# Kernel tuning notes

Hardware: AMD Instinct MI355X
Metric: run time of the kernel (lower is better)

## Reference

```python
import jax, jax.numpy as jnp
import numpy as np

B, T, I, H, O = 128, 1024, 256, 1024, 128


def setup_inputs() -> dict:
    key = jax.random.key(0)
    ks = jax.random.split(key, 7)
    s = 1.0 / np.sqrt(H)  # PyTorch GRUCell init scale
    return {
        "sequence": jax.random.normal(ks[0], (B, T, I), dtype=jnp.float32),
        "W_ih": jax.random.uniform(ks[1], (3 * H, I), jnp.float32, -s, s),
        "W_hh": jax.random.uniform(ks[2], (3 * H, H), jnp.float32, -s, s),
        "b_ih": jax.random.uniform(ks[3], (3 * H,), jnp.float32, -s, s),
        "b_hh": jax.random.uniform(ks[4], (3 * H,), jnp.float32, -s, s),
        "W_out": jax.random.uniform(ks[5], (O, H), jnp.float32, -s, s),
        "b_out": jax.random.uniform(ks[6], (O,), jnp.float32, -s, s),
    }


def reference(sequence, W_ih, W_hh, b_ih, b_hh, W_out, b_out):
    Bs, Ts, _ = sequence.shape
    Hs = W_hh.shape[1]

    def step(h, x_t):
        gi = x_t @ W_ih.T + b_ih            # [B, 3H]
        gh = h @ W_hh.T + b_hh              # [B, 3H]
        i_r, i_z, i_n = jnp.split(gi, 3, axis=1)
        h_r, h_z, h_n = jnp.split(gh, 3, axis=1)
        r = jax.nn.sigmoid(i_r + h_r)
        z = jax.nn.sigmoid(i_z + h_z)
        n = jnp.tanh(i_n + r * h_n)
        h_new = (1.0 - z) * n + z * h       # PyTorch GRUCell update
        out = jax.nn.log_softmax(h_new @ W_out.T + b_out, axis=1)
        return h_new, out

    xs = jnp.swapaxes(sequence[:, : Ts - 1, :], 0, 1)  # [T-1, B, I]
    h0 = jnp.zeros((Bs, Hs), dtype=sequence.dtype)     # init_hx = zeros
    _, outs = jax.lax.scan(step, h0, xs)               # [T-1, B, O]
    return jnp.swapaxes(outs, 0, 1)                    # [B, T-1, O]
```

## Files before the change

### kernel.cpp

```cpp
#include <hip/hip_runtime.h>


typedef __attribute__((ext_vector_type(8))) __bf16 bf16x8;
typedef __attribute__((ext_vector_type(4))) float floatx4;
typedef __attribute__((ext_vector_type(8))) unsigned short ushortx8;
typedef unsigned short ushort_t;
typedef unsigned int uint_t;
typedef unsigned long long ull_t;

#define T_ 1024
#define I_ 256

#define NWPACK   3932160
#define NWOPACK  131072
#define HPACK_SLOT 131072
#define WPACK_OFF   0
#define WOPACK_OFF  (NWPACK*2)
#define HPACK_OFF   (WOPACK_OFF + NWOPACK*2)
#define OUTPART_OFF (HPACK_OFF + 4*HPACK_SLOT*2)
#define BAR_OFF     (OUTPART_OFF + 131072*4)

__device__ __forceinline__ ushort_t f2bf(float f) {
    uint_t u = __float_as_uint(f);
    u += 0x7fffu + ((u >> 16) & 1u);
    return (ushort_t)(u >> 16);
}

__device__ __forceinline__ floatx4 mfma16(bf16x8 a, bf16x8 b, floatx4 c) {
    return __builtin_amdgcn_mfma_f32_16x16x32_bf16(a, b, c, 0, 0, 0);
}

__device__ __forceinline__ bf16x8 ld_llc16(const ushort_t* p) {
    union { ull_t q[2]; bf16x8 v; } u;
    u.q[0] = __hip_atomic_load((const ull_t*)p,     __ATOMIC_RELAXED, __HIP_MEMORY_SCOPE_AGENT);
    u.q[1] = __hip_atomic_load((const ull_t*)p + 1, __ATOMIC_RELAXED, __HIP_MEMORY_SCOPE_AGENT);
    return u.v;
}
__device__ __forceinline__ void st_llc2(ushort_t* p, ushort_t v) {
    __hip_atomic_store(p, v, __ATOMIC_RELAXED, __HIP_MEMORY_SCOPE_AGENT);
}
__device__ __forceinline__ void st_llc4f(float* p, float v) {
    __hip_atomic_store(p, v, __ATOMIC_RELAXED, __HIP_MEMORY_SCOPE_AGENT);
}
__device__ __forceinline__ float ld_llc4f(const float* p) {
    return __hip_atomic_load(p, __ATOMIC_RELAXED, __HIP_MEMORY_SCOPE_AGENT);
}

__global__ void gru_init(const float* __restrict__ W_ih, const float* __restrict__ W_hh,
                         const float* __restrict__ W_out,
                         ushort_t* __restrict__ wpack, ushort_t* __restrict__ wopack,
                         ushort_t* __restrict__ hpack0, uint_t* __restrict__ bar)
{
    const int total = NWPACK + NWOPACK + HPACK_SLOT/2 + 1024;
    for (int e = blockIdx.x * 256 + threadIdx.x; e < total; e += gridDim.x * 256) {
        if (e < NWPACK) {
            int j = e & 7;
            int lane = (e >> 3) & 63;
            int t2 = e >> 9;
            int g  = t2 % 3;
            int t3 = t2 / 3;
            int kb = t3 % 40;
            int cg = t3 / 40;
            int n = g * 1024 + cg * 16 + (lane & 15);
            int koff = ((lane >> 4) << 3) + j;
            float v;
            if (kb < 8) v = W_ih[(size_t)n * 256 + kb * 32 + koff];
            else        v = W_hh[(size_t)n * 1024 + (kb - 8) * 32 + koff];
            wpack[e] = f2bf(v);
        } else if (e < NWPACK + NWOPACK) {
            int e2 = e - NWPACK;
            int j = e2 & 7;
            int lane = (e2 >> 3) & 63;
            int kb = (e2 >> 9) & 31;
            int nt = e2 >> 14;
            int n = nt * 16 + (lane & 15);
            int k = kb * 32 + ((lane >> 4) << 3) + j;
            wopack[e2] = f2bf(W_out[(size_t)n * 1024 + k]);
        } else if (e < NWPACK + NWOPACK + HPACK_SLOT/2) {
            ((uint_t*)hpack0)[e - NWPACK - NWOPACK] = 0u;
        } else {
            bar[e - NWPACK - NWOPACK - HPACK_SLOT/2] = 0u;
        }
    }
}

__device__ __forceinline__ void group_barrier(uint_t* bar, int grp, uint_t target)
{
    __syncthreads();
    if (threadIdx.x == 0) {
        uint_t* cnt = bar + grp * 64;
        uint_t* gen = bar + grp * 64 + 32;
        uint_t a = __hip_atomic_fetch_add(cnt, 1u, __ATOMIC_RELAXED, __HIP_MEMORY_SCOPE_AGENT);
        if (a == (target << 6) - 1u) {
            __hip_atomic_fetch_add(gen, 1u, __ATOMIC_RELAXED, __HIP_MEMORY_SCOPE_AGENT);
        } else {
            while (__hip_atomic_load(gen, __ATOMIC_RELAXED, __HIP_MEMORY_SCOPE_AGENT) < target)
                __builtin_amdgcn_s_sleep(1);
        }
    }
    __syncthreads();
}

__global__ void __launch_bounds__(256, 1)
gru_main(const float* __restrict__ seq,
         const float* __restrict__ b_ih, const float* __restrict__ b_hh,
         const float* __restrict__ b_out,
         const ushort_t* __restrict__ wpack, const ushort_t* __restrict__ wopack,
         ushort_t* __restrict__ hpack, float* __restrict__ outpart,
         uint_t* __restrict__ bar, float* __restrict__ dout)
{
    extern __shared__ char lds[];
    ushort_t* wlds = (ushort_t*)lds;
    float*    xch  = (float*)(lds + 122880);

    const int b   = blockIdx.x;
    const int grp = (b & 7) >> 1;
    const int id  = ((b >> 3) << 1) | (b & 1);
    const int cg  = id;
    const int m   = grp;
    const int tid = threadIdx.x;
    const int wv  = tid >> 6;
    const int ln  = tid & 63;

    {
        const uint4* src = (const uint4*)(wpack + (size_t)cg * 61440);
        uint4* dst = (uint4*)lds;
        for (int i = tid; i < 7680; i += 256) dst[i] = src[i];
    }

    float bihr = 0, bhhr = 0, bihz = 0, bhhz = 0, bihn = 0, bhhn = 0;
    if (wv < 2) {
        int col = cg * 16 + (ln & 15);
        bihr = b_ih[col];          bhhr = b_hh[col];
        bihz = b_ih[1024 + col];   bhhz = b_hh[1024 + col];
        bihn = b_ih[2048 + col];   bhhn = b_hh[2048 + col];
    }
    const float bo0 = b_out[ln], bo1 = b_out[ln + 64];

    floatx4 hold = {0.f, 0.f, 0.f, 0.f};

    const int omt = 2 * grp + (id & 1);
    const int ont = (id >> 1) & 7;
    const int oks = (id >> 4) & 3;
    const int kb0 = wv * 10;
    const int mtb0 = m * 2, mtb1 = m * 2 + 1;

    __syncthreads();

#define XSLOT(sw, mt, g) (xch + (((sw) * 2 + (mt)) * 4 + (g)) * 256 + ln * 4)

    for (int it = 0; it < 1025; ++it) {
        const ushort_t* hcur = hpack + (size_t)(it & 3) * HPACK_SLOT;

        floatx4 accr0 = {0,0,0,0}, accr1 = {0,0,0,0};
        floatx4 accz0 = {0,0,0,0}, accz1 = {0,0,0,0};
        floatx4 acch0 = {0,0,0,0}, acch1 = {0,0,0,0};
        floatx4 acci0 = {0,0,0,0}, acci1 = {0,0,0,0};

        if (it <= 1022) {
            #pragma unroll
            for (int ki = 0; ki < 10; ++ki) {
                const int kb = kb0 + ki;
                bf16x8 a0, a1;
                if (kb < 8) {
                    int koffx = kb * 32 + ((ln >> 4) << 3);
                    const float* p0 = seq + (size_t)(mtb0 * 16 + (ln & 15)) * (T_ * I_)
                                          + (size_t)it * I_ + koffx;
                    const float* p1 = p0 + (size_t)16 * (T_ * I_);
                    float4 fa = *(const float4*)p0, fb = *(const float4*)(p0 + 4);
                    float4 ga = *(const float4*)p1, gb = *(const float4*)(p1 + 4);
                    ushortx8 u0, u1;
                    u0[0] = f2bf(fa.x); u0[1] = f2bf(fa.y); u0[2] = f2bf(fa.z); u0[3] = f2bf(fa.w);
                    u0[4] = f2bf(fb.x); u0[5] = f2bf(fb.y); u0[6] = f2bf(fb.z); u0[7] = f2bf(fb.w);
                    u1[0] = f2bf(ga.x); u1[1] = f2bf(ga.y); u1[2] = f2bf(ga.z); u1[3] = f2bf(ga.w);
                    u1[4] = f2bf(gb.x); u1[5] = f2bf(gb.y); u1[6] = f2bf(gb.z); u1[7] = f2bf(gb.w);
                    a0 = __builtin_bit_cast(bf16x8, u0);
                    a1 = __builtin_bit_cast(bf16x8, u1);
                } else {
                    a0 = ld_llc16(hcur + (((size_t)mtb0 * 32 + (kb - 8)) * 64 + ln) * 8);
                    a1 = ld_llc16(hcur + (((size_t)mtb1 * 32 + (kb - 8)) * 64 + ln) * 8);
                }
                const bf16x8 br = *(const bf16x8*)(wlds + ((kb * 3 + 0) * 64 + ln) * 8);
                const bf16x8 bz = *(const bf16x8*)(wlds + ((kb * 3 + 1) * 64 + ln) * 8);
                const bf16x8 bn = *(const bf16x8*)(wlds + ((kb * 3 + 2) * 64 + ln) * 8);
                accr0 = mfma16(a0, br, accr0);  accr1 = mfma16(a1, br, accr1);
                accz0 = mfma16(a0, bz, accz0);  accz1 = mfma16(a1, bz, accz1);
                if (kb < 8) { acci0 = mfma16(a0, bn, acci0); acci1 = mfma16(a1, bn, acci1); }
                else        { acch0 = mfma16(a0, bn, acch0); acch1 = mfma16(a1, bn, acch1); }
            }
            if (wv == 0) {
                *(floatx4*)XSLOT(0, 1, 0) = accr1; *(floatx4*)XSLOT(0, 1, 1) = accz1;
                *(floatx4*)XSLOT(0, 1, 2) = acch1; *(floatx4*)XSLOT(0, 1, 3) = acci1;
            } else if (wv == 1) {
                *(floatx4*)XSLOT(1, 0, 0) = accr0; *(floatx4*)XSLOT(1, 0, 1) = accz0;
                *(floatx4*)XSLOT(1, 0, 2) = acch0;
            } else {
                *(floatx4*)XSLOT(wv, 0, 0) = accr0; *(floatx4*)XSLOT(wv, 0, 1) = accz0;
                *(floatx4*)XSLOT(wv, 0, 2) = acch0;
                *(floatx4*)XSLOT(wv, 1, 0) = accr1; *(floatx4*)XSLOT(wv, 1, 1) = accz1;
                *(floatx4*)XSLOT(wv, 1, 2) = acch1;
            }
        }
        __syncthreads();

        if (it <= 1022 && wv < 2) {
            const int mtr = wv;
            floatx4 r  = (mtr == 0) ? accr0 : accr1;
            floatx4 z  = (mtr == 0) ? accz0 : accz1;
            floatx4 hn = (mtr == 0) ? acch0 : acch1;
            floatx4 inn = (wv == 0) ? acci0 : *(floatx4*)XSLOT(0, 1, 3);
            #pragma unroll
            for (int sw = 0; sw < 4; ++sw) {
                if (sw == wv) continue;
                r  += *(floatx4*)XSLOT(sw, mtr, 0);
                z  += *(floatx4*)XSLOT(sw, mtr, 1);
                hn += *(floatx4*)XSLOT(sw, mtr, 2);
            }
            ushort_t* hnew = hpack + (size_t)((it + 1) & 3) * HPACK_SLOT;
            const int mtW = m * 2 + mtr;
            const int kbh = cg >> 1;
            const int koffb = ((cg & 1) << 4) + (ln & 15);
            const int lanep = (koffb >> 3) << 4;
            const int jj = koffb & 7;
            const int rbase = (ln >> 4) * 4;
            #pragma unroll
            for (int e = 0; e < 4; ++e) {
                float rp = r[e] + bihr + bhhr;
                float rg = 1.f / (1.f + __expf(-rp));
                float zp = z[e] + bihz + bhhz;
                float zg = 1.f / (1.f + __expf(-zp));
                float nx = inn[e] + bihn + rg * (hn[e] + bhhn);
                float ng = 1.f - 2.f / (__expf(2.f * nx) + 1.f);
                float hv = (1.f - zg) * ng + zg * hold[e];
                hold[e] = hv;
                size_t idx = (((size_t)mtW * 32 + kbh) * 64 + (unsigned)((rbase + e) | lanep)) * 8 + jj;
                st_llc2(&hnew[idx], f2bf(hv));
            }
        }

        if (wv == 2 && it >= 1 && it <= 1023) {
            const ushort_t* hh = hpack + (size_t)(it & 3) * HPACK_SLOT;
            floatx4 acc = {0, 0, 0, 0};
            #pragma unroll
            for (int i2 = 0; i2 < 8; ++i2) {
                int kb = oks * 8 + i2;
                bf16x8 a = ld_llc16(hh + (((size_t)omt * 32 + kb) * 64 + ln) * 8);
                bf16x8 bb = *(const bf16x8*)(wopack + (((size_t)ont * 32 + kb) * 64 + ln) * 8);
                acc = mfma16(a, bb, acc);
            }
            float* op = outpart + (size_t)(it & 1) * 65536 + (size_t)oks * 16384;
            int colo = ont * 16 + (ln & 15);
            #pragma unroll
            for (int e = 0; e < 4; ++e) {
                int rowo = omt * 16 + (ln >> 4) * 4 + e;
                st_llc4f(op + rowo * 128 + colo, acc[e]);
            }
        }

        if (wv == 3 && id < 32 && it >= 2) {
            const float* op = outpart + (size_t)((it - 1) & 1) * 65536;
            const int row = grp * 32 + id;
            float v0 = bo0, v1 = bo1;
            #pragma unroll
            for (int ks2 = 0; ks2 < 4; ++ks2) {
                v0 += ld_llc4f(op + ks2 * 16384 + row * 128 + ln);
                v1 += ld_llc4f(op + ks2 * 16384 + row * 128 + ln + 64);
            }
            float mx = fmaxf(v0, v1);
            #pragma unroll
            for (int off = 32; off >= 1; off >>= 1) mx = fmaxf(mx, __shfl_xor(mx, off));
            float e0 = __expf(v0 - mx), e1 = __expf(v1 - mx);
            float sm = e0 + e1;
            #pragma unroll
            for (int off = 32; off >= 1; off >>= 1) sm += __shfl_xor(sm, off);
            float lse = mx + __logf(sm);
            float* po = dout + ((size_t)row * 1023 + (it - 2)) * 128;
            po[ln] = v0 - lse;
            po[ln + 64] = v1 - lse;
        }

        if (it < 1024) group_barrier(bar, grp, (uint_t)(it + 1));
    }
#undef XSLOT
}

extern "C" void kernel_launch(void* const* d_in, const int* in_sizes, int n_in,
                              void* d_out, int out_size, void* d_ws, size_t ws_size,
                              hipStream_t stream)
{
    const float* seq  = (const float*)d_in[0];
    const float* Wih  = (const float*)d_in[1];
    const float* Whh  = (const float*)d_in[2];
    const float* bih  = (const float*)d_in[3];
    const float* bhh  = (const float*)d_in[4];
    const float* Wout = (const float*)d_in[5];
    const float* bout = (const float*)d_in[6];

    char* ws = (char*)d_ws;
    ushort_t* wpack   = (ushort_t*)(ws + WPACK_OFF);
    ushort_t* wopack  = (ushort_t*)(ws + WOPACK_OFF);
    ushort_t* hpack   = (ushort_t*)(ws + HPACK_OFF);
    float*    outpart = (float*)(ws + OUTPART_OFF);
    uint_t*   bar     = (uint_t*)(ws + BAR_OFF);

    gru_init<<<1024, 256, 0, stream>>>(Wih, Whh, Wout, wpack, wopack, hpack, bar);

    hipFuncSetAttribute((const void*)gru_main,
                        hipFuncAttributeMaxDynamicSharedMemorySize, 155648);
    gru_main<<<256, 256, 155648, stream>>>(seq, bih, bhh, bout, wpack, wopack,
                                           hpack, outpart, bar, (float*)d_out);
}
```

Baseline: 9.504 ms.

## Replace group barrier with per-wave counter waits and overlap input projection

Replaces the full block-level group barrier with a monotonically increasing per-group counter: the two gate waves increment it after their hidden-state stores drain, and every wave polls it individually only before consuming the new hidden state. The input-projection MFMAs and the output-projection partials are hoisted ahead of the wait, so they overlap with the cross-block synchronization. The new hidden state is staged in LDS and written as 64-bit stores instead of scattered 16-bit stores. The output pipeline is deepened to four buffers to tolerate the looser coupling. The cost is extra LDS space and more complex memory-ordering assumptions, with relaxed atomics and an explicit vmcnt wait.

```diff
diff --git a/kernel.cpp b/kernel.cpp
--- a/kernel.cpp
+++ b/kernel.cpp
@@ -18,7 +18,7 @@
 #define WOPACK_OFF  (NWPACK*2)
 #define HPACK_OFF   (WOPACK_OFF + NWOPACK*2)
 #define OUTPART_OFF (HPACK_OFF + 4*HPACK_SLOT*2)
-#define BAR_OFF     (OUTPART_OFF + 131072*4)
+#define BAR_OFF     (OUTPART_OFF + 4*65536*4)
 
 __device__ __forceinline__ ushort_t f2bf(float f) {
     uint_t u = __float_as_uint(f);
@@ -36,7 +36,7 @@
     u.q[1] = __hip_atomic_load((const ull_t*)p + 1, __ATOMIC_RELAXED, __HIP_MEMORY_SCOPE_AGENT);
     return u.v;
 }
-__device__ __forceinline__ void st_llc2(ushort_t* p, ushort_t v) {
+__device__ __forceinline__ void st_llc8(ull_t* p, ull_t v) {
     __hip_atomic_store(p, v, __ATOMIC_RELAXED, __HIP_MEMORY_SCOPE_AGENT);
 }
 __device__ __forceinline__ void st_llc4f(float* p, float v) {
@@ -84,21 +84,14 @@
     }
 }
 
-__device__ __forceinline__ void group_barrier(uint_t* bar, int grp, uint_t target)
+__device__ __forceinline__ void wave_wait(uint_t* cnt, uint_t target, int ln)
 {
-    __syncthreads();
-    if (threadIdx.x == 0) {
-        uint_t* cnt = bar + grp * 64;
-        uint_t* gen = bar + grp * 64 + 32;
-        uint_t a = __hip_atomic_fetch_add(cnt, 1u, __ATOMIC_RELAXED, __HIP_MEMORY_SCOPE_AGENT);
-        if (a == (target << 6) - 1u) {
-            __hip_atomic_fetch_add(gen, 1u, __ATOMIC_RELAXED, __HIP_MEMORY_SCOPE_AGENT);
-        } else {
-            while (__hip_atomic_load(gen, __ATOMIC_RELAXED, __HIP_MEMORY_SCOPE_AGENT) < target)
-                __builtin_amdgcn_s_sleep(1);
-        }
-    }
-    __syncthreads();
+    if (ln == 0) {
+        while (__hip_atomic_load(cnt, __ATOMIC_RELAXED, __HIP_MEMORY_SCOPE_AGENT) < target)
+            __builtin_amdgcn_s_sleep(1);
+    }
+    __builtin_amdgcn_wave_barrier();
+    asm volatile("" ::: "memory");
 }
 
 __global__ void __launch_bounds__(256, 1)
@@ -112,6 +105,7 @@
     extern __shared__ char lds[];
     ushort_t* wlds = (ushort_t*)lds;
     float*    xch  = (float*)(lds + 122880);
+    ushort_t* hsc  = (ushort_t*)(lds + 155648);
 
     const int b   = blockIdx.x;
     const int grp = (b & 7) >> 1;
@@ -121,6 +115,7 @@
     const int tid = threadIdx.x;
     const int wv  = tid >> 6;
     const int ln  = tid & 63;
+    uint_t* cnt = bar + grp * 64;
 
     {
         const uint4* src = (const uint4*)(wpack + (size_t)cg * 61440);
@@ -142,16 +137,13 @@
     const int omt = 2 * grp + (id & 1);
     const int ont = (id >> 1) & 7;
     const int oks = (id >> 4) & 3;
-    const int kb0 = wv * 10;
     const int mtb0 = m * 2, mtb1 = m * 2 + 1;
 
     __syncthreads();
 
 #define XSLOT(sw, mt, g) (xch + (((sw) * 2 + (mt)) * 4 + (g)) * 256 + ln * 4)
 
-    for (int it = 0; it < 1025; ++it) {
-        const ushort_t* hcur = hpack + (size_t)(it & 3) * HPACK_SLOT;
-
+    for (int it = 0; it < 1026; ++it) {
         floatx4 accr0 = {0,0,0,0}, accr1 = {0,0,0,0};
         floatx4 accz0 = {0,0,0,0}, accz1 = {0,0,0,0};
         floatx4 acch0 = {0,0,0,0}, acch1 = {0,0,0,0};
@@ -159,47 +151,91 @@
 
         if (it <= 1022) {
             #pragma unroll
-            for (int ki = 0; ki < 10; ++ki) {
-                const int kb = kb0 + ki;
-                bf16x8 a0, a1;
-                if (kb < 8) {
-                    int koffx = kb * 32 + ((ln >> 4) << 3);
-                    const float* p0 = seq + (size_t)(mtb0 * 16 + (ln & 15)) * (T_ * I_)
-                                          + (size_t)it * I_ + koffx;
-                    const float* p1 = p0 + (size_t)16 * (T_ * I_);
-                    float4 fa = *(const float4*)p0, fb = *(const float4*)(p0 + 4);
-                    float4 ga = *(const float4*)p1, gb = *(const float4*)(p1 + 4);
-                    ushortx8 u0, u1;
-                    u0[0] = f2bf(fa.x); u0[1] = f2bf(fa.y); u0[2] = f2bf(fa.z); u0[3] = f2bf(fa.w);
-                    u0[4] = f2bf(fb.x); u0[5] = f2bf(fb.y); u0[6] = f2bf(fb.z); u0[7] = f2bf(fb.w);
-                    u1[0] = f2bf(ga.x); u1[1] = f2bf(ga.y); u1[2] = f2bf(ga.z); u1[3] = f2bf(ga.w);
-                    u1[4] = f2bf(gb.x); u1[5] = f2bf(gb.y); u1[6] = f2bf(gb.z); u1[7] = f2bf(gb.w);
-                    a0 = __builtin_bit_cast(bf16x8, u0);
-                    a1 = __builtin_bit_cast(bf16x8, u1);
-                } else {
-                    a0 = ld_llc16(hcur + (((size_t)mtb0 * 32 + (kb - 8)) * 64 + ln) * 8);
-                    a1 = ld_llc16(hcur + (((size_t)mtb1 * 32 + (kb - 8)) * 64 + ln) * 8);
-                }
+            for (int ki = 0; ki < 2; ++ki) {
+                const int kb = wv * 2 + ki;
+                int koffx = kb * 32 + ((ln >> 4) << 3);
+                const float* p0 = seq + (size_t)(mtb0 * 16 + (ln & 15)) * (T_ * I_)
+                                      + (size_t)it * I_ + koffx;
+                const float* p1 = p0 + (size_t)16 * (T_ * I_);
+                float4 fa = *(const float4*)p0, fb = *(const float4*)(p0 + 4);
+                float4 ga = *(const float4*)p1, gb = *(const float4*)(p1 + 4);
+                ushortx8 u0, u1;
+                u0[0] = f2bf(fa.x); u0[1] = f2bf(fa.y); u0[2] = f2bf(fa.z); u0[3] = f2bf(fa.w);
+                u0[4] = f2bf(fb.x); u0[5] = f2bf(fb.y); u0[6] = f2bf(fb.z); u0[7] = f2bf(fb.w);
+                u1[0] = f2bf(ga.x); u1[1] = f2bf(ga.y); u1[2] = f2bf(ga.z); u1[3] = f2bf(ga.w);
+                u1[4] = f2bf(gb.x); u1[5] = f2bf(gb.y); u1[6] = f2bf(gb.z); u1[7] = f2bf(gb.w);
+                bf16x8 a0 = __builtin_bit_cast(bf16x8, u0);
+                bf16x8 a1 = __builtin_bit_cast(bf16x8, u1);
                 const bf16x8 br = *(const bf16x8*)(wlds + ((kb * 3 + 0) * 64 + ln) * 8);
                 const bf16x8 bz = *(const bf16x8*)(wlds + ((kb * 3 + 1) * 64 + ln) * 8);
                 const bf16x8 bn = *(const bf16x8*)(wlds + ((kb * 3 + 2) * 64 + ln) * 8);
                 accr0 = mfma16(a0, br, accr0);  accr1 = mfma16(a1, br, accr1);
                 accz0 = mfma16(a0, bz, accz0);  accz1 = mfma16(a1, bz, accz1);
-                if (kb < 8) { acci0 = mfma16(a0, bn, acci0); acci1 = mfma16(a1, bn, acci1); }
-                else        { acch0 = mfma16(a0, bn, acch0); acch1 = mfma16(a1, bn, acch1); }
-            }
-            if (wv == 0) {
-                *(floatx4*)XSLOT(0, 1, 0) = accr1; *(floatx4*)XSLOT(0, 1, 1) = accz1;
-                *(floatx4*)XSLOT(0, 1, 2) = acch1; *(floatx4*)XSLOT(0, 1, 3) = acci1;
-            } else if (wv == 1) {
-                *(floatx4*)XSLOT(1, 0, 0) = accr0; *(floatx4*)XSLOT(1, 0, 1) = accz0;
-                *(floatx4*)XSLOT(1, 0, 2) = acch0;
-            } else {
-                *(floatx4*)XSLOT(wv, 0, 0) = accr0; *(floatx4*)XSLOT(wv, 0, 1) = accz0;
-                *(floatx4*)XSLOT(wv, 0, 2) = acch0;
-                *(floatx4*)XSLOT(wv, 1, 0) = accr1; *(floatx4*)XSLOT(wv, 1, 1) = accz1;
-                *(floatx4*)XSLOT(wv, 1, 2) = acch1;
-            }
+                acci0 = mfma16(a0, bn, acci0);  acci1 = mfma16(a1, bn, acci1);
+            }
+        }
+
+        if (wv == 2 && it >= 2 && it <= 1024) {
+            const ushort_t* hh = hpack + (size_t)((it - 1) & 3) * HPACK_SLOT;
+            floatx4 acc = {0, 0, 0, 0};
+            #pragma unroll
+            for (int i2 = 0; i2 < 8; ++i2) {
+                int kb = oks * 8 + i2;
+                bf16x8 a = ld_llc16(hh + (((size_t)omt * 32 + kb) * 64 + ln) * 8);
+                bf16x8 bb = *(const bf16x8*)(wopack + (((size_t)ont * 32 + kb) * 64 + ln) * 8);
+                acc = mfma16(a, bb, acc);
+            }
+            float* op = outpart + (size_t)(it & 3) * 65536 + (size_t)oks * 16384;
+            int colo = ont * 16 + (ln & 15);
+            #pragma unroll
+            for (int e = 0; e < 4; ++e) {
+                int rowo = omt * 16 + (ln >> 4) * 4 + e;
+                st_llc4f(op + rowo * 128 + colo, acc[e]);
+            }
+        }
+
+        wave_wait(cnt, (uint_t)it * 128u, ln);
+
+        if (wv == 3 && id < 32 && it >= 3) {
+            const float* op = outpart + (size_t)((it - 1) & 3) * 65536;
+            const int row = grp * 32 + id;
+            float v0 = bo0, v1 = bo1;
+            #pragma unroll
+            for (int ks2 = 0; ks2 < 4; ++ks2) {
+                v0 += ld_llc4f(op + ks2 * 16384 + row * 128 + ln);
+                v1 += ld_llc4f(op + ks2 * 16384 + row * 128 + ln + 64);
+            }
+            float mx = fmaxf(v0, v1);
+            #pragma unroll
+            for (int off = 32; off >= 1; off >>= 1) mx = fmaxf(mx, __shfl_xor(mx, off));
+            float e0 = __expf(v0 - mx), e1 = __expf(v1 - mx);
+            float sm = e0 + e1;
+            #pragma unroll
+            for (int off = 32; off >= 1; off >>= 1) sm += __shfl_xor(sm, off);
+            float lse = mx + __logf(sm);
+            float* po = dout + ((size_t)row * 1023 + (it - 3)) * 128;
+            po[ln] = v0 - lse;
+            po[ln + 64] = v1 - lse;
+        }
+
+        if (it <= 1022) {
+            const ushort_t* hcur = hpack + (size_t)(it & 3) * HPACK_SLOT;
+            #pragma unroll
+            for (int ki = 0; ki < 8; ++ki) {
+                const int kb = 8 + wv * 8 + ki;
+                bf16x8 a0 = ld_llc16(hcur + (((size_t)mtb0 * 32 + (kb - 8)) * 64 + ln) * 8);
+                bf16x8 a1 = ld_llc16(hcur + (((size_t)mtb1 * 32 + (kb - 8)) * 64 + ln) * 8);
+                const bf16x8 br = *(const bf16x8*)(wlds + ((kb * 3 + 0) * 64 + ln) * 8);
+                const bf16x8 bz = *(const bf16x8*)(wlds + ((kb * 3 + 1) * 64 + ln) * 8);
+                const bf16x8 bn = *(const bf16x8*)(wlds + ((kb * 3 + 2) * 64 + ln) * 8);
+                accr0 = mfma16(a0, br, accr0);  accr1 = mfma16(a1, br, accr1);
+                accz0 = mfma16(a0, bz, accz0);  accz1 = mfma16(a1, bz, accz1);
+                acch0 = mfma16(a0, bn, acch0);  acch1 = mfma16(a1, bn, acch1);
+            }
+            *(floatx4*)XSLOT(wv, 0, 0) = accr0; *(floatx4*)XSLOT(wv, 0, 1) = accz0;
+            *(floatx4*)XSLOT(wv, 0, 2) = acch0; *(floatx4*)XSLOT(wv, 0, 3) = acci0;
+            *(floatx4*)XSLOT(wv, 1, 0) = accr1; *(floatx4*)XSLOT(wv, 1, 1) = accz1;
+            *(floatx4*)XSLOT(wv, 1, 2) = acch1; *(floatx4*)XSLOT(wv, 1, 3) = acci1;
         }
         __syncthreads();
 
@@ -208,21 +244,18 @@
             floatx4 r  = (mtr == 0) ? accr0 : accr1;
             floatx4 z  = (mtr == 0) ? accz0 : accz1;
             floatx4 hn = (mtr == 0) ? acch0 : acch1;
-            floatx4 inn = (wv == 0) ? acci0 : *(floatx4*)XSLOT(0, 1, 3);
+            floatx4 inn = (mtr == 0) ? acci0 : acci1;
             #pragma unroll
             for (int sw = 0; sw < 4; ++sw) {
                 if (sw == wv) continue;
-                r  += *(floatx4*)XSLOT(sw, mtr, 0);
-                z  += *(floatx4*)XSLOT(sw, mtr, 1);
-                hn += *(floatx4*)XSLOT(sw, mtr, 2);
-            }
-            ushort_t* hnew = hpack + (size_t)((it + 1) & 3) * HPACK_SLOT;
-            const int mtW = m * 2 + mtr;
-            const int kbh = cg >> 1;
-            const int koffb = ((cg & 1) << 4) + (ln & 15);
-            const int lanep = (koffb >> 3) << 4;
-            const int jj = koffb & 7;
+                r   += *(floatx4*)XSLOT(sw, mtr, 0);
+                z   += *(floatx4*)XSLOT(sw, mtr, 1);
+                hn  += *(floatx4*)XSLOT(sw, mtr, 2);
+                inn += *(floatx4*)XSLOT(sw, mtr, 3);
+            }
+            const int cwithin = ln & 15;
             const int rbase = (ln >> 4) * 4;
+            ushort_t* sc = hsc + mtr * 256;
             #pragma unroll
             for (int e = 0; e < 4; ++e) {
                 float rp = r[e] + bihr + bhhr;
@@ -233,53 +266,27 @@
                 float ng = 1.f - 2.f / (__expf(2.f * nx) + 1.f);
                 float hv = (1.f - zg) * ng + zg * hold[e];
                 hold[e] = hv;
-                size_t idx = (((size_t)mtW * 32 + kbh) * 64 + (unsigned)((rbase + e) | lanep)) * 8 + jj;
-                st_llc2(&hnew[idx], f2bf(hv));
-            }
-        }
-
-        if (wv == 2 && it >= 1 && it <= 1023) {
-            const ushort_t* hh = hpack + (size_t)(it & 3) * HPACK_SLOT;
-            floatx4 acc = {0, 0, 0, 0};
-            #pragma unroll
-            for (int i2 = 0; i2 < 8; ++i2) {
-                int kb = oks * 8 + i2;
-                bf16x8 a = ld_llc16(hh + (((size_t)omt * 32 + kb) * 64 + ln) * 8);
-                bf16x8 bb = *(const bf16x8*)(wopack + (((size_t)ont * 32 + kb) * 64 + ln) * 8);
-                acc = mfma16(a, bb, acc);
-            }
-            float* op = outpart + (size_t)(it & 1) * 65536 + (size_t)oks * 16384;
-            int colo = ont * 16 + (ln & 15);
-            #pragma unroll
-            for (int e = 0; e < 4; ++e) {
-                int rowo = omt * 16 + (ln >> 4) * 4 + e;
-                st_llc4f(op + rowo * 128 + colo, acc[e]);
-            }
-        }
-
-        if (wv == 3 && id < 32 && it >= 2) {
-            const float* op = outpart + (size_t)((it - 1) & 1) * 65536;
-            const int row = grp * 32 + id;
-            float v0 = bo0, v1 = bo1;
-            #pragma unroll
-            for (int ks2 = 0; ks2 < 4; ++ks2) {
-                v0 += ld_llc4f(op + ks2 * 16384 + row * 128 + ln);
-                v1 += ld_llc4f(op + ks2 * 16384 + row * 128 + ln + 64);
-            }
-            float mx = fmaxf(v0, v1);
-            #pragma unroll
-            for (int off = 32; off >= 1; off >>= 1) mx = fmaxf(mx, __shfl_xor(mx, off));
-            float e0 = __expf(v0 - mx), e1 = __expf(v1 - mx);
-            float sm = e0 + e1;
-            #pragma unroll
-            for (int off = 32; off >= 1; off >>= 1) sm += __shfl_xor(sm, off);
-            float lse = mx + __logf(sm);
-            float* po = dout + ((size_t)row * 1023 + (it - 2)) * 128;
-            po[ln] = v0 - lse;
-            po[ln + 64] = v1 - lse;
-        }
-
-        if (it < 1024) group_barrier(bar, grp, (uint_t)(it + 1));
+                sc[((cwithin >> 3) * 16 + rbase + e) * 8 + (cwithin & 7)] = f2bf(hv);
+            }
+            __builtin_amdgcn_wave_barrier();
+            if (ln < 32) {
+                const ull_t* q = (const ull_t*)(sc) + ln * 2;
+                ull_t q0 = q[0], q1 = q[1];
+                const int mtW = m * 2 + mtr;
+                const int kbh = cg >> 1;
+                const int base_lane = (cg & 1) * 32;
+                ushort_t* hnew = hpack + (size_t)((it + 1) & 3) * HPACK_SLOT;
+                ull_t* p = (ull_t*)(hnew + (((size_t)mtW * 32 + kbh) * 64 + base_lane + ln) * 8);
+                st_llc8(p, q0);
+                st_llc8(p + 1, q1);
+            }
+        }
+
+        if (wv < 2 && it <= 1024) {
+            if (it <= 1022) asm volatile("s_waitcnt vmcnt(0)" ::: "memory");
+            if (ln == 0)
+                __hip_atomic_fetch_add(cnt, 1u, __ATOMIC_RELAXED, __HIP_MEMORY_SCOPE_AGENT);
+        }
     }
 #undef XSLOT
 }
@@ -306,7 +313,7 @@
     gru_init<<<1024, 256, 0, stream>>>(Wih, Whh, Wout, wpack, wopack, hpack, bar);
 
     hipFuncSetAttribute((const void*)gru_main,
-                        hipFuncAttributeMaxDynamicSharedMemorySize, 155648);
-    gru_main<<<256, 256, 155648, stream>>>(seq, bih, bhh, bout, wpack, wopack,
+                        hipFuncAttributeMaxDynamicSharedMemorySize, 156672);
+    gru_main<<<256, 256, 156672, stream>>>(seq, bih, bhh, bout, wpack, wopack,
                                            hpack, outpart, bar, (float*)d_out);
 }
```

Measured after the change: 11.96 ms. 25.8% more time.
